# Kernel tuning notes

Measured on AMD Instinct MI355X. Metric: run time of the kernel, lower is better.

Reference implementation:

```python
import jax, jax.numpy as jnp
import numpy as np
from itertools import permutations

N = 4            # n_streams
C = 2048         # hidden_size
NC = N * C
NFACT = 24       # 4!
DFF = 4 * C
B, S = 2, 4096
EPS = 1.1920929e-07  # torch F.rms_norm default eps = finfo(fp32).eps


def _perm_mat():
    perms = list(permutations(range(N)))
    P = np.zeros((len(perms), N * N), np.float32)
    for i, p in enumerate(perms):
        for r, c in enumerate(p):
            P[i, r * N + c] = 1.0
    return jnp.asarray(P)


def setup_inputs() -> dict:
    key = jax.random.key(0)
    ks = jax.random.split(key, 8)
    total_out = 2 * N + NFACT
    return {
        "x_streams": jax.random.normal(ks[0], (B, S, N, C), jnp.float32),
        "W_all": jax.random.normal(ks[1], (total_out, NC), jnp.float32) * (1.0 / np.sqrt(NC)),
        "b_all": jax.random.normal(ks[2], (total_out,), jnp.float32) * 0.02,
        "alpha_pre": jnp.array([0.01], jnp.float32),
        "alpha_post": jnp.array([0.01], jnp.float32),
        "alpha_res": jnp.array([0.01], jnp.float32),
        "W1": jax.random.normal(ks[3], (DFF, C), jnp.float32) * (1.0 / np.sqrt(C)),
        "b1": jnp.zeros((DFF,), jnp.float32),
        "W2": jax.random.normal(ks[4], (C, DFF), jnp.float32) * (1.0 / np.sqrt(DFF)),
        "b2": jnp.zeros((C,), jnp.float32),
        "perm_mat": _perm_mat(),
    }


def reference(x_streams, W_all, b_all, alpha_pre, alpha_post, alpha_res, W1, b1, W2, b2, perm_mat):
    # --- coefficients: fused RMSNorm + projection + gating ---
    x_flat = x_streams.reshape(*x_streams.shape[:-2], NC)            # (B,S,nC)
    x_norm = x_flat * jax.lax.rsqrt(jnp.mean(x_flat * x_flat, axis=-1, keepdims=True) + EPS)
    all_proj = x_norm @ W_all.T                                       # (B,S,2n+n!)
    pre_proj = all_proj[..., :N]
    post_proj = all_proj[..., N:2 * N]
    res_proj = all_proj[..., 2 * N:]
    h_pre = jax.nn.sigmoid(alpha_pre * pre_proj + b_all[:N])          # (B,S,n)
    h_post = 2.0 * jax.nn.sigmoid(alpha_post * post_proj + b_all[N:2 * N])
    a_res = jax.nn.softmax(alpha_res * res_proj + b_all[2 * N:], axis=-1)  # (B,S,n!)
    H_res = (a_res @ perm_mat).reshape(*a_res.shape[:-1], N, N)       # (B,S,n,n)
    H_merged = H_res - h_post[..., :, None] * h_pre[..., None, :]
    # --- pre-map: weighted sum over streams ---
    layer_input = jnp.einsum('bsn,bsnc->bsc', h_pre, x_streams)       # (B,S,C)
    # --- wrapped layer: GELU MLP (no residual) ---
    h = jax.nn.gelu(layer_input @ W1.T + b1, approximate=False)
    layer_output = h @ W2.T + b2                                      # (B,S,C)
    # --- post-res mixing ---
    out = jnp.einsum('bsij,bsjc->bsic', H_merged, x_streams) \
        + h_post[..., None] * layer_output[..., None, :]
    return out
```

## Files before the change

kernel.cpp:

```cpp
#include <hip/hip_runtime.h>
#include <hip/hip_bf16.h>
#include <math.h>

#define NC_DIM 8192
#define C_DIM 2048
#define NTOK 8192
#define EPS_RMS 1.1920929e-07f

typedef __bf16 bf16_t;
typedef __attribute__((ext_vector_type(8))) __bf16 bf16x8;
typedef __attribute__((ext_vector_type(4))) __bf16 bf16x4;
typedef __attribute__((ext_vector_type(4))) float f32x4;

__device__ __forceinline__ void gload_lds16(const void* g, void* l) {
    __builtin_amdgcn_global_load_lds(
        (const __attribute__((address_space(1))) void*)g,
        (__attribute__((address_space(3))) void*)l, 16, 0, 0);
}

__global__ __launch_bounds__(256) void cvt_f32_bf16(const float* __restrict__ in,
                                                    bf16_t* __restrict__ out,
                                                    const int n4) {
    int i = blockIdx.x * 256 + threadIdx.x;
    const int stride = gridDim.x * 256;
    for (; i < n4; i += stride) {
        f32x4 v = ((const f32x4*)in)[i];
        bf16x4 bv;
        bv.x = (__bf16)v.x; bv.y = (__bf16)v.y; bv.z = (__bf16)v.z; bv.w = (__bf16)v.w;
        ((bf16x4*)out)[i] = bv;
    }
}

__global__ __launch_bounds__(256) void k_proj(
    const float* __restrict__ x,
    const float* __restrict__ Wall,
    const float* __restrict__ ball,
    const float* __restrict__ apre,
    const float* __restrict__ apost,
    const float* __restrict__ ares,
    const float* __restrict__ perm,
    float* __restrict__ hpre_g,
    float* __restrict__ hpost_g,
    float* __restrict__ Hm_g)
{
    __shared__ __align__(16) bf16_t xs[32 * 264];
    __shared__ __align__(16) bf16_t wsl[32 * 264];
    __shared__ float dparts[4][32][32];
    __shared__ float ssq_s[32];
    __shared__ float Ps[384];

    const int t = threadIdx.x;
    const int lane = t & 63;
    const int w = t >> 6;
    const int tok0 = blockIdx.x * 32;

    for (int i = t; i < 384; i += 256) Ps[i] = perm[i];

    const int row = t >> 3;
    const int i8 = t & 7;

    const float* xrow = x + (size_t)(tok0 + row) * (size_t)NC_DIM;
    const float* wrow = Wall + (size_t)row * (size_t)NC_DIM;

    float ssq = 0.0f;
    f32x4 acc[2][2];
#pragma unroll
    for (int m = 0; m < 2; ++m)
#pragma unroll
        for (int n = 0; n < 2; ++n) acc[m][n] = (f32x4){0.f, 0.f, 0.f, 0.f};

    const int rsel = lane & 15;
    const int ko_base = (lane >> 4) * 8;

    for (int kt = 0; kt < NC_DIM; kt += 256) {
        __syncthreads();
#pragma unroll
        for (int q = 0; q < 8; ++q) {
            const int col = (i8 + q * 8) * 4;
            f32x4 v = *(const f32x4*)(xrow + kt + col);
            ssq += v.x * v.x + v.y * v.y + v.z * v.z + v.w * v.w;
            bf16x4 bv;
            bv.x = (__bf16)v.x; bv.y = (__bf16)v.y; bv.z = (__bf16)v.z; bv.w = (__bf16)v.w;
            *(bf16x4*)(xs + row * 264 + col) = bv;
            f32x4 u = *(const f32x4*)(wrow + kt + col);
            bf16x4 bu;
            bu.x = (__bf16)u.x; bu.y = (__bf16)u.y; bu.z = (__bf16)u.z; bu.w = (__bf16)u.w;
            *(bf16x4*)(wsl + row * 264 + col) = bu;
        }
        __syncthreads();
#pragma unroll
        for (int ks = 0; ks < 2; ++ks) {
            const int ko = w * 64 + ks * 32 + ko_base;
            bf16x8 a0 = *(const bf16x8*)(xs + rsel * 264 + ko);
            bf16x8 a1 = *(const bf16x8*)(xs + (16 + rsel) * 264 + ko);
            bf16x8 b0 = *(const bf16x8*)(wsl + rsel * 264 + ko);
            bf16x8 b1 = *(const bf16x8*)(wsl + (16 + rsel) * 264 + ko);
            acc[0][0] = __builtin_amdgcn_mfma_f32_16x16x32_bf16(a0, b0, acc[0][0], 0, 0, 0);
            acc[0][1] = __builtin_amdgcn_mfma_f32_16x16x32_bf16(a0, b1, acc[0][1], 0, 0, 0);
            acc[1][0] = __builtin_amdgcn_mfma_f32_16x16x32_bf16(a1, b0, acc[1][0], 0, 0, 0);
            acc[1][1] = __builtin_amdgcn_mfma_f32_16x16x32_bf16(a1, b1, acc[1][1], 0, 0, 0);
        }
    }

    ssq += __shfl_xor(ssq, 1);
    ssq += __shfl_xor(ssq, 2);
    ssq += __shfl_xor(ssq, 4);
    if (i8 == 0) ssq_s[row] = ssq;

    const int cr = (lane >> 4) * 4;
#pragma unroll
    for (int m = 0; m < 2; ++m)
#pragma unroll
        for (int n = 0; n < 2; ++n)
#pragma unroll
            for (int j = 0; j < 4; ++j)
                dparts[w][m * 16 + cr + j][n * 16 + rsel] = acc[m][n][j];
    __syncthreads();

    if (t < 32) {
        const int g = tok0 + t;
        const float rinv = rsqrtf(ssq_s[t] * (1.0f / (float)NC_DIM) + EPS_RMS);
        float proj[32];
#pragma unroll
        for (int r = 0; r < 32; ++r)
            proj[r] = (dparts[0][t][r] + dparts[1][t][r] + dparts[2][t][r] + dparts[3][t][r]) * rinv;
        const float aP = apre[0], aQ = apost[0], aR = ares[0];
        float hp[4], hq[4];
#pragma unroll
        for (int i = 0; i < 4; ++i) {
            hp[i] = 1.0f / (1.0f + expf(-(aP * proj[i] + __ldg(&ball[i]))));
            hq[i] = 2.0f / (1.0f + expf(-(aQ * proj[4 + i] + __ldg(&ball[4 + i]))));
        }
        float zb[24];
        float mx = -1e30f;
#pragma unroll
        for (int p = 0; p < 24; ++p) {
            zb[p] = aR * proj[8 + p] + __ldg(&ball[8 + p]);
            mx = fmaxf(mx, zb[p]);
        }
        float s = 0.f;
#pragma unroll
        for (int p = 0; p < 24; ++p) { zb[p] = expf(zb[p] - mx); s += zb[p]; }
        const float is = 1.0f / s;
        float Hr[16];
#pragma unroll
        for (int idx = 0; idx < 16; ++idx) Hr[idx] = 0.f;
#pragma unroll
        for (int p = 0; p < 24; ++p) {
            const float a = zb[p] * is;
#pragma unroll
            for (int idx = 0; idx < 16; ++idx) Hr[idx] += a * Ps[p * 16 + idx];
        }
#pragma unroll
        for (int i = 0; i < 4; ++i) {
            hpre_g[(size_t)g * 4 + i] = hp[i];
            hpost_g[(size_t)g * 4 + i] = hq[i];
#pragma unroll
            for (int j = 0; j < 4; ++j)
                Hm_g[(size_t)g * 16 + i * 4 + j] = Hr[i * 4 + j] - hq[i] * hp[j];
        }
    }
}

__global__ __launch_bounds__(256) void k_mix(
    const float* __restrict__ x,
    const float* __restrict__ hpre_g,
    bf16_t* __restrict__ li)
{
    __shared__ float hp[8][4];
    const int t = threadIdx.x;
    const size_t tok0 = (size_t)blockIdx.x * 8;
    if (t < 32) hp[t >> 2][t & 3] = hpre_g[tok0 * 4 + t];
    __syncthreads();
    const int tl = t >> 5;
    const int ci = (t & 31) * 4;
    const size_t g = tok0 + tl;
    const float* xb = x + g * (size_t)NC_DIM;
    bf16_t* lo = li + g * (size_t)C_DIM;
    const float h0 = hp[tl][0], h1 = hp[tl][1], h2 = hp[tl][2], h3 = hp[tl][3];
#pragma unroll
    for (int q = 0; q < 16; ++q) {
        const int c = ci + q * 128;
        f32x4 v0 = *(const f32x4*)(xb + c);
        f32x4 v1 = *(const f32x4*)(xb + 2048 + c);
        f32x4 v2 = *(const f32x4*)(xb + 4096 + c);
        f32x4 v3 = *(const f32x4*)(xb + 6144 + c);
        f32x4 r = h0 * v0 + h1 * v1 + h2 * v2 + h3 * v3;
        bf16x4 bv;
        bv.x = (__bf16)r.x; bv.y = (__bf16)r.y; bv.z = (__bf16)r.z; bv.w = (__bf16)r.w;
        *(bf16x4*)(lo + c) = bv;
    }
}

template <int MODE>
__global__ __launch_bounds__(512, 2) void gemm8(
    const bf16_t* __restrict__ A,
    const bf16_t* __restrict__ Bm,
    const float* __restrict__ bias,
    void* __restrict__ Cout,
    const int M, const int N, const int K)
{
    __shared__ __align__(16) char lds[131072];
    const int tid = threadIdx.x;
    const int lane = tid & 63;
    const int w = tid >> 6;
    const int wr = w >> 2;
    const int wc = w & 3;

    const int nbn = N >> 8;
    const int cpx = gridDim.x >> 3;
    const int bid = blockIdx.x;
    const int swz = (bid & 7) * cpx + (bid >> 3);
    const long tm = (long)(swz / nbn) * 256;
    const long tn = (long)(swz % nbn) * 256;

    const int NT = K >> 6;

    const int rsel = lane & 15;
    const int ko = (lane >> 4) * 8;
    const int lane_off = rsel * 64 + ((ko ^ (((rsel >> 1) & 3) << 3)) << 1);

    const char* Abytes = (const char*)A;
    const char* Bbytes = (const char*)Bm;
    size_t asrc[2][2], bsrc[2][2];
#pragma unroll
    for (int i = 0; i < 2; ++i) {
        const int d = i * 8192 + tid * 16;
        {
            const int awr = d >> 13, rem = d & 8191;
            const int sub = rem >> 10, rs = sub >> 1, ksub = sub & 1;
            const int rr = (rem >> 6) & 15;
            const int kk = ((rem & 63) >> 1) ^ (((rr >> 1) & 3) << 3);
            const int k = ksub * 32 + kk;
#pragma unroll
            for (int mq = 0; mq < 2; ++mq) {
                const long grow = tm + awr * 128 + mq * 64 + rs * 16 + rr;
                asrc[mq][i] = ((size_t)grow * K + k) * 2;
            }
        }
        {
            const int bwc = d >> 12, rem = d & 4095;
            const int sub = rem >> 10, rs = sub >> 1, ksub = sub & 1;
            const int rr = (rem >> 6) & 15;
            const int kk = ((rem & 63) >> 1) ^ (((rr >> 1) & 3) << 3);
            const int k = ksub * 32 + kk;
#pragma unroll
            for (int np = 0; np < 2; ++np) {
                const long grow = tn + bwc * 64 + np * 32 + rs * 16 + rr;
                bsrc[np][i] = ((size_t)grow * K + k) * 2;
            }
        }
    }

    auto stageA = [&](int mq, int tile, int slot) {
        const int tt = tile < NT ? tile : NT - 1;
        char* dst = lds + slot * 65536 + mq * 16384 + w * 1024;
        gload_lds16(Abytes + asrc[mq][0] + (size_t)tt * 128, dst);
        gload_lds16(Abytes + asrc[mq][1] + (size_t)tt * 128, dst + 8192);
    };
    auto stageB = [&](int np, int tile, int slot) {
        const int tt = tile < NT ? tile : NT - 1;
        char* dst = lds + slot * 65536 + 32768 + np * 16384 + w * 1024;
        gload_lds16(Bbytes + bsrc[np][0] + (size_t)tt * 128, dst);
        gload_lds16(Bbytes + bsrc[np][1] + (size_t)tt * 128, dst + 8192);
    };

    const char* aB = lds + wr * 8192;
    const char* bB = lds + 32768 + wc * 4096;

    f32x4 acc[8][4];
#pragma unroll
    for (int m = 0; m < 8; ++m)
#pragma unroll
        for (int n = 0; n < 4; ++n) acc[m][n] = (f32x4){0.f, 0.f, 0.f, 0.f};

    bf16x8 aR[4][2], b01[2][2], b23[2][2];

    auto readA = [&](const char* aS, int off) {
#pragma unroll
        for (int mf = 0; mf < 4; ++mf)
#pragma unroll
            for (int ks = 0; ks < 2; ++ks)
                aR[mf][ks] = *(const bf16x8*)(aS + off + (mf * 2 + ks) * 1024 + lane_off);
    };
    auto readB = [&](bf16x8 (&bf)[2][2], const char* bS, int off) {
#pragma unroll
        for (int nf = 0; nf < 2; ++nf)
#pragma unroll
            for (int ks = 0; ks < 2; ++ks)
                bf[nf][ks] = *(const bf16x8*)(bS + off + (nf * 2 + ks) * 1024 + lane_off);
    };

#define MFMA_Q(MBASE, NBASE, BF)                                                   \
    __builtin_amdgcn_s_setprio(1);                                                 \
    _Pragma("unroll")                                                              \
    for (int ks = 0; ks < 2; ++ks)                                                 \
        _Pragma("unroll")                                                          \
        for (int mf = 0; mf < 4; ++mf)                                             \
            _Pragma("unroll")                                                      \
            for (int nf = 0; nf < 2; ++nf)                                         \
                acc[(MBASE) + mf][(NBASE) + nf] =                                  \
                    __builtin_amdgcn_mfma_f32_16x16x32_bf16(                       \
                        aR[mf][ks], BF[nf][ks], acc[(MBASE) + mf][(NBASE) + nf],   \
                        0, 0, 0);                                                  \
    __builtin_amdgcn_s_setprio(0);

#define BAR() __builtin_amdgcn_s_barrier()
#define LGKM0() asm volatile("s_waitcnt lgkmcnt(0)" ::: "memory")
#define LGKM8() asm volatile("s_waitcnt lgkmcnt(8)" ::: "memory")
#define VM6() asm volatile("s_waitcnt vmcnt(6)" ::: "memory")

    stageA(0, 0, 0); stageB(0, 0, 0); stageB(1, 0, 0); stageA(1, 0, 0);
    stageA(0, 1, 1); stageB(0, 1, 1); stageB(1, 1, 1);
    VM6();
    BAR();

    const int NI = NT >> 1;
    for (int it = 0; it < NI; ++it) {
        const int T = it * 2;
        const char* aS0 = aB;
        const char* bS0 = bB;
        const char* aS1 = aB + 65536;
        const char* bS1 = bB + 65536;

        readA(aS0, 0);
        readB(b01, bS0, 0);
        stageA(1, T + 1, 1);
        LGKM8();
        BAR(); LGKM0();
        MFMA_Q(0, 0, b01)
        BAR();
        readB(b23, bS0, 16384);
        stageA(0, T + 2, 0);
        BAR(); LGKM0();
        MFMA_Q(0, 2, b23)
        BAR();
        readA(aS0, 16384);
        stageB(0, T + 2, 0);
        BAR(); LGKM0();
        MFMA_Q(4, 2, b23)
        BAR();
        stageB(1, T + 2, 0);
        VM6();
        BAR();
        MFMA_Q(4, 0, b01)
        BAR();
        readA(aS1, 0);
        readB(b01, bS1, 0);
        stageA(1, T + 2, 0);
        LGKM8();
        BAR(); LGKM0();
        MFMA_Q(0, 0, b01)
        BAR();
        readB(b23, bS1, 16384);
        stageA(0, T + 3, 1);
        BAR(); LGKM0();
        MFMA_Q(0, 2, b23)
        BAR();
        readA(aS1, 16384);
        stageB(0, T + 3, 1);
        BAR(); LGKM0();
        MFMA_Q(4, 2, b23)
        BAR();
        stageB(1, T + 3, 1);
        VM6();
        BAR();
        MFMA_Q(4, 0, b01)
        BAR();
    }
#undef MFMA_Q
#undef BAR
#undef LGKM0
#undef LGKM8
#undef VM6

#pragma unroll
    for (int mq = 0; mq < 2; ++mq)
#pragma unroll
        for (int mf = 0; mf < 4; ++mf) {
            const long rbase = tm + wr * 128 + mq * 64 + mf * 16 + (lane >> 4) * 4;
#pragma unroll
            for (int np = 0; np < 2; ++np)
#pragma unroll
                for (int nf = 0; nf < 2; ++nf) {
                    const long cg = tn + wc * 64 + np * 32 + nf * 16 + rsel;
                    const float bv = __ldg(&bias[cg]);
                    const f32x4 v4 = acc[mq * 4 + mf][np * 2 + nf];
#pragma unroll
                    for (int j = 0; j < 4; ++j) {
                        const float v = v4[j] + bv;
                        if (MODE == 0) {
                            const float ge = 0.5f * v * (1.0f + erff(v * 0.70710678118654752f));
                            ((bf16_t*)Cout)[(size_t)(rbase + j) * N + cg] = (__bf16)ge;
                        } else {
                            ((float*)Cout)[(size_t)(rbase + j) * N + cg] = v;
                        }
                    }
                }
        }
}

__global__ __launch_bounds__(256) void k_final(
    const float* __restrict__ x,
    const float* __restrict__ LO,
    const float* __restrict__ hpost_g,
    const float* __restrict__ Hm_g,
    float* __restrict__ out)
{
    __shared__ float Hm[16];
    __shared__ float hp[4];
    const int t = threadIdx.x;
    const size_t g = blockIdx.x;
    if (t < 16) Hm[t] = Hm_g[g * 16 + t];
    if (t >= 16 && t < 20) hp[t - 16] = hpost_g[g * 4 + (t - 16)];
    __syncthreads();
    const float* xb = x + g * (size_t)NC_DIM;
    const float* lob = LO + g * (size_t)C_DIM;
    float* ob = out + g * (size_t)NC_DIM;
#pragma unroll
    for (int q = 0; q < 2; ++q) {
        const int c = t * 4 + q * 1024;
        f32x4 x0 = *(const f32x4*)(xb + c);
        f32x4 x1 = *(const f32x4*)(xb + 2048 + c);
        f32x4 x2 = *(const f32x4*)(xb + 4096 + c);
        f32x4 x3 = *(const f32x4*)(xb + 6144 + c);
        f32x4 l4 = *(const f32x4*)(lob + c);
#pragma unroll
        for (int i = 0; i < 4; ++i) {
            f32x4 r = Hm[i * 4 + 0] * x0 + Hm[i * 4 + 1] * x1 + Hm[i * 4 + 2] * x2 +
                      Hm[i * 4 + 3] * x3 + hp[i] * l4;
            *(f32x4*)(ob + i * 2048 + c) = r;
        }
    }
}

extern "C" void kernel_launch(void* const* d_in, const int* in_sizes, int n_in,
                              void* d_out, int out_size, void* d_ws, size_t ws_size,
                              hipStream_t stream) {
    const float* x     = (const float*)d_in[0];
    const float* Wall  = (const float*)d_in[1];
    const float* ball  = (const float*)d_in[2];
    const float* apre  = (const float*)d_in[3];
    const float* apost = (const float*)d_in[4];
    const float* ares  = (const float*)d_in[5];
    const float* W1    = (const float*)d_in[6];
    const float* b1    = (const float*)d_in[7];
    const float* W2    = (const float*)d_in[8];
    const float* b2    = (const float*)d_in[9];
    const float* perm  = (const float*)d_in[10];
    float* out = (float*)d_out;
    char* ws = (char*)d_ws;

    bf16_t* W1b  = (bf16_t*)(ws);
    bf16_t* W2b  = (bf16_t*)(ws + 33554432ull);
    bf16_t* li   = (bf16_t*)(ws + 67108864ull);
    bf16_t* h    = (bf16_t*)(ws + 100663296ull);
    float*  LO   = (float*)(ws + 234881024ull);
    float*  hpre = (float*)(ws + 301989888ull);
    float*  hpost= (float*)(ws + 302120960ull);
    float*  Hm   = (float*)(ws + 302252032ull);

    cvt_f32_bf16<<<2048, 256, 0, stream>>>(W1, W1b, 16777216 / 4);
    cvt_f32_bf16<<<2048, 256, 0, stream>>>(W2, W2b, 16777216 / 4);
    k_proj<<<256, 256, 0, stream>>>(x, Wall, ball, apre, apost, ares, perm, hpre, hpost, Hm);
    k_mix<<<1024, 256, 0, stream>>>(x, hpre, li);
    gemm8<0><<<1024, 512, 0, stream>>>(li, W1b, b1, (void*)h, 8192, 8192, 2048);
    gemm8<1><<<256, 512, 0, stream>>>(h, W2b, b2, (void*)LO, 8192, 2048, 8192);
    k_final<<<8192, 256, 0, stream>>>(x, LO, hpost, Hm, out);
}
```

Before: 829.4 us.

## Double-buffer LDS fragment registers to overlap LDS reads with MFMA

Adds a second set of A and B register fragments so that LDS reads for the next MFMA quadrant are issued before the current quadrant's MFMAs run. It drops the explicit lgkmcnt waits in favour of sched_barrier and compiler-inserted waits, and halves the number of barriers per step. The goal is to hide LDS read latency behind matrix math. In exchange it raises VGPR pressure, which may lower occupancy, and the reduced barriers and explicit waits risk a stale read or race if the tile ordering is not exactly right.

```diff
diff --git a/kernel.cpp b/kernel.cpp
--- a/kernel.cpp
+++ b/kernel.cpp
@@ -267,6 +267,10 @@
 
     const char* aB = lds + wr * 8192;
     const char* bB = lds + 32768 + wc * 4096;
+    const char* aS0 = aB;
+    const char* bS0 = bB;
+    const char* aS1 = aB + 65536;
+    const char* bS1 = bB + 65536;
 
     f32x4 acc[8][4];
 #pragma unroll
@@ -274,24 +278,24 @@
 #pragma unroll
         for (int n = 0; n < 4; ++n) acc[m][n] = (f32x4){0.f, 0.f, 0.f, 0.f};
 
-    bf16x8 aR[4][2], b01[2][2], b23[2][2];
-
-    auto readA = [&](const char* aS, int off) {
+    bf16x8 aX[4][2], aY[4][2], b01X[2][2], b01Y[2][2], b23[2][2];
+
+    auto readA = [&](bf16x8 (&ar)[4][2], const char* base) {
 #pragma unroll
         for (int mf = 0; mf < 4; ++mf)
 #pragma unroll
             for (int ks = 0; ks < 2; ++ks)
-                aR[mf][ks] = *(const bf16x8*)(aS + off + (mf * 2 + ks) * 1024 + lane_off);
+                ar[mf][ks] = *(const bf16x8*)(base + (mf * 2 + ks) * 1024 + lane_off);
     };
-    auto readB = [&](bf16x8 (&bf)[2][2], const char* bS, int off) {
+    auto readB2 = [&](bf16x8 (&bf)[2][2], const char* base) {
 #pragma unroll
         for (int nf = 0; nf < 2; ++nf)
 #pragma unroll
             for (int ks = 0; ks < 2; ++ks)
-                bf[nf][ks] = *(const bf16x8*)(bS + off + (nf * 2 + ks) * 1024 + lane_off);
+                bf[nf][ks] = *(const bf16x8*)(base + (nf * 2 + ks) * 1024 + lane_off);
     };
 
-#define MFMA_Q(MBASE, NBASE, BF)                                                   \
+#define MFMA_Q(MB, NB, AR, BF)                                                     \
     __builtin_amdgcn_s_setprio(1);                                                 \
     _Pragma("unroll")                                                              \
     for (int ks = 0; ks < 2; ++ks)                                                 \
@@ -299,80 +303,75 @@
         for (int mf = 0; mf < 4; ++mf)                                             \
             _Pragma("unroll")                                                      \
             for (int nf = 0; nf < 2; ++nf)                                         \
-                acc[(MBASE) + mf][(NBASE) + nf] =                                  \
+                acc[(MB) + mf][(NB) + nf] =                                        \
                     __builtin_amdgcn_mfma_f32_16x16x32_bf16(                       \
-                        aR[mf][ks], BF[nf][ks], acc[(MBASE) + mf][(NBASE) + nf],   \
+                        AR[mf][ks], BF[nf][ks], acc[(MB) + mf][(NB) + nf],         \
                         0, 0, 0);                                                  \
     __builtin_amdgcn_s_setprio(0);
 
 #define BAR() __builtin_amdgcn_s_barrier()
-#define LGKM0() asm volatile("s_waitcnt lgkmcnt(0)" ::: "memory")
-#define LGKM8() asm volatile("s_waitcnt lgkmcnt(8)" ::: "memory")
 #define VM6() asm volatile("s_waitcnt vmcnt(6)" ::: "memory")
+#define SCHED0() __builtin_amdgcn_sched_barrier(0)
 
     stageA(0, 0, 0); stageB(0, 0, 0); stageB(1, 0, 0); stageA(1, 0, 0);
     stageA(0, 1, 1); stageB(0, 1, 1); stageB(1, 1, 1);
     VM6();
     BAR();
+    readA(aX, aS0);
+    readB2(b01X, bS0);
 
     const int NI = NT >> 1;
     for (int it = 0; it < NI; ++it) {
         const int T = it * 2;
-        const char* aS0 = aB;
-        const char* bS0 = bB;
-        const char* aS1 = aB + 65536;
-        const char* bS1 = bB + 65536;
-
-        readA(aS0, 0);
-        readB(b01, bS0, 0);
+        BAR();
         stageA(1, T + 1, 1);
-        LGKM8();
-        BAR(); LGKM0();
-        MFMA_Q(0, 0, b01)
-        BAR();
-        readB(b23, bS0, 16384);
+        readB2(b23, bS0 + 16384);
+        SCHED0();
+        MFMA_Q(0, 0, aX, b01X)
+        BAR();
         stageA(0, T + 2, 0);
-        BAR(); LGKM0();
-        MFMA_Q(0, 2, b23)
-        BAR();
-        readA(aS0, 16384);
+        VM6();
+        readA(aY, aS0 + 16384);
+        SCHED0();
+        MFMA_Q(0, 2, aX, b23)
+        BAR();
         stageB(0, T + 2, 0);
-        BAR(); LGKM0();
-        MFMA_Q(4, 2, b23)
+        readA(aX, aS1);
+        readB2(b01Y, bS1);
+        SCHED0();
+        MFMA_Q(4, 2, aY, b23)
         BAR();
         stageB(1, T + 2, 0);
         VM6();
-        BAR();
-        MFMA_Q(4, 0, b01)
-        BAR();
-        readA(aS1, 0);
-        readB(b01, bS1, 0);
+        SCHED0();
+        MFMA_Q(4, 0, aY, b01X)
+        BAR();
         stageA(1, T + 2, 0);
-        LGKM8();
-        BAR(); LGKM0();
-        MFMA_Q(0, 0, b01)
-        BAR();
-        readB(b23, bS1, 16384);
+        readB2(b23, bS1 + 16384);
+        SCHED0();
+        MFMA_Q(0, 0, aX, b01Y)
+        BAR();
         stageA(0, T + 3, 1);
-        BAR(); LGKM0();
-        MFMA_Q(0, 2, b23)
-        BAR();
-        readA(aS1, 16384);
+        VM6();
+        readA(aY, aS1 + 16384);
+        SCHED0();
+        MFMA_Q(0, 2, aX, b23)
+        BAR();
         stageB(0, T + 3, 1);
-        BAR(); LGKM0();
-        MFMA_Q(4, 2, b23)
+        readA(aX, aS0);
+        readB2(b01X, bS0);
+        SCHED0();
+        MFMA_Q(4, 2, aY, b23)
         BAR();
         stageB(1, T + 3, 1);
         VM6();
-        BAR();
-        MFMA_Q(4, 0, b01)
-        BAR();
+        SCHED0();
+        MFMA_Q(4, 0, aY, b01Y)
     }
 #undef MFMA_Q
 #undef BAR
-#undef LGKM0
-#undef LGKM8
 #undef VM6
+#undef SCHED0
 
 #pragma unroll
     for (int mq = 0; mq < 2; ++mq)
```

Result: slower. 1.914 ms (+130.8%).
